# Optimization experiments

Measured on AMD Instinct MI355X. Metric: run time of the kernel, lower is better.

## Reference

```python
import jax, jax.numpy as jnp
import numpy as np

B, D = 65536, 512
E_SPEC, E_SH = 2, 2
H1, H2, EO, TH = 64, 32, 32, 64
T1_DIM, T2_DIM = 3, 2


def _lin(key, shape, fan_in):
    bound = 1.0 / np.sqrt(fan_in)
    return jax.random.uniform(key, shape, jnp.float32, -bound, bound)


def _expert_params(key, n):
    ks = jax.random.split(key, 6)
    return (
        _lin(ks[0], (n, D, H1), D), _lin(ks[1], (n, H1), D),
        _lin(ks[2], (n, H1, H2), H1), _lin(ks[3], (n, H2), H1),
        _lin(ks[4], (n, H2, EO), H2), _lin(ks[5], (n, EO), H2),
    )


def setup_inputs() -> dict:
    key = jax.random.key(0)
    ks = jax.random.split(key, 8)
    x = jax.random.normal(ks[0], (B, D), jnp.float32)
    sh = _expert_params(ks[1], E_SH)
    t1 = _expert_params(ks[2], E_SPEC)
    t2 = _expert_params(ks[3], E_SPEC)
    EG = E_SPEC + E_SH
    g1_W, g1_b = _lin(jax.random.fold_in(ks[4], 0), (D, EG), D), _lin(jax.random.fold_in(ks[4], 1), (EG,), D)
    g2_W, g2_b = _lin(jax.random.fold_in(ks[5], 0), (D, EG), D), _lin(jax.random.fold_in(ks[5], 1), (EG,), D)
    kt = jax.random.split(ks[6], 4)
    tw1_W1, tw1_b1 = _lin(kt[0], (EO, TH), EO), _lin(kt[1], (TH,), EO)
    tw1_W2, tw1_b2 = _lin(kt[2], (TH, T1_DIM), TH), _lin(kt[3], (T1_DIM,), TH)
    kt2 = jax.random.split(ks[7], 4)
    tw2_W1, tw2_b1 = _lin(kt2[0], (EO, TH), EO), _lin(kt2[1], (TH,), EO)
    tw2_W2, tw2_b2 = _lin(kt2[2], (TH, T2_DIM), TH), _lin(kt2[3], (T2_DIM,), TH)
    return {
        "x": x,
        "sh_W1": sh[0], "sh_b1": sh[1], "sh_W2": sh[2], "sh_b2": sh[3], "sh_W3": sh[4], "sh_b3": sh[5],
        "t1_W1": t1[0], "t1_b1": t1[1], "t1_W2": t1[2], "t1_b2": t1[3], "t1_W3": t1[4], "t1_b3": t1[5],
        "t2_W1": t2[0], "t2_b1": t2[1], "t2_W2": t2[2], "t2_b2": t2[3], "t2_W3": t2[4], "t2_b3": t2[5],
        "g1_W": g1_W, "g1_b": g1_b, "g2_W": g2_W, "g2_b": g2_b,
        "tw1_W1": tw1_W1, "tw1_b1": tw1_b1, "tw1_W2": tw1_W2, "tw1_b2": tw1_b2,
        "tw2_W1": tw2_W1, "tw2_b1": tw2_b1, "tw2_W2": tw2_W2, "tw2_b2": tw2_b2,
    }


def _experts(x, W1, b1, W2, b2, W3, b3):
    # batched over expert dim e: [e, B, h] (dropout is identity in eval)
    h = jax.nn.relu(jnp.einsum('bi,eih->ebh', x, W1) + b1[:, None, :])
    h = jax.nn.relu(jnp.einsum('ebh,ehk->ebk', h, W2) + b2[:, None, :])
    return jnp.einsum('ebk,eko->ebo', h, W3) + b3[:, None, :]


def _tower(g, W1, b1, W2, b2):
    return jax.nn.relu(g @ W1 + b1) @ W2 + b2


def reference(x, sh_W1, sh_b1, sh_W2, sh_b2, sh_W3, sh_b3,
              t1_W1, t1_b1, t1_W2, t1_b2, t1_W3, t1_b3,
              t2_W1, t2_b1, t2_W2, t2_b2, t2_W3, t2_b3,
              g1_W, g1_b, g2_W, g2_b,
              tw1_W1, tw1_b1, tw1_W2, tw1_b2,
              tw2_W1, tw2_b1, tw2_W2, tw2_b2):
    shared = _experts(x, sh_W1, sh_b1, sh_W2, sh_b2, sh_W3, sh_b3)   # [E_SH, B, EO]
    task1 = _experts(x, t1_W1, t1_b1, t1_W2, t1_b2, t1_W3, t1_b3)    # [E_SPEC, B, EO]
    task2 = _experts(x, t2_W1, t2_b1, t2_W2, t2_b2, t2_W3, t2_b3)

    sel1 = jax.nn.softmax(x @ g1_W + g1_b, axis=1)                    # [B, E_SPEC+E_SH]
    g1 = jnp.einsum('ebc,be->bc', jnp.concatenate([task1, shared], 0), sel1)
    o1 = _tower(g1, tw1_W1, tw1_b1, tw1_W2, tw1_b2)
    o1 = o1.at[:, 0].set(jax.nn.sigmoid(o1[:, 0]))
    o1 = o1.at[:, 2].set(jax.nn.sigmoid(o1[:, 2]))

    sel2 = jax.nn.softmax(x @ g2_W + g2_b, axis=1)
    g2 = jnp.einsum('ebc,be->bc', jnp.concatenate([task2, shared], 0), sel2)
    o2 = _tower(g2, tw2_W1, tw2_b1, tw2_W2, tw2_b2)
    o2 = o2.at[:, 1].set(jax.nn.sigmoid(o2[:, 1]))
    return (o1, o2)
```

## Files before the change

### kernel.cpp

```cpp
#include <hip/hip_runtime.h>
#include <hip/hip_bf16.h>


#define MT 64
#define NT1 25

typedef __bf16 bf16x8 __attribute__((ext_vector_type(8)));
typedef float f32x4 __attribute__((ext_vector_type(4)));

__device__ __forceinline__ unsigned short f2bf(float f) {
    unsigned u = __builtin_bit_cast(unsigned, f);
    return (unsigned short)((u + 0x7FFFu + ((u >> 16) & 1u)) >> 16);
}

__global__ void pack_w1(const float* __restrict__ sh_W1, const float* __restrict__ t1_W1,
                        const float* __restrict__ t2_W1, const float* __restrict__ g1_W,
                        const float* __restrict__ g2_W, unsigned short* __restrict__ wf1) {
    int p = blockIdx.x * blockDim.x + threadIdx.x;
    if (p >= NT1 * 16 * 64 * 8) return;
    int j = p & 7, lane = (p >> 3) & 63, ks = (p >> 9) & 15, nt = p >> 13;
    int col = nt * 16 + (lane & 15);
    int k = ks * 32 + (lane >> 4) * 8 + j;
    float v = 0.f;
    if (col < 384) {
        int e = col >> 6, ci = col & 63;
        const float* W = (e < 2) ? t1_W1 : (e < 4) ? t2_W1 : sh_W1;
        v = W[((size_t)(e & 1) * 512 + k) * 64 + ci];
    } else if (col < 388) {
        v = g1_W[k * 4 + (col - 384)];
    } else if (col < 392) {
        v = g2_W[k * 4 + (col - 388)];
    }
    wf1[p] = f2bf(v);
}

__global__ void pack_rest(const float* __restrict__ sh_W2, const float* __restrict__ t1_W2,
                          const float* __restrict__ t2_W2,
                          const float* __restrict__ sh_W3, const float* __restrict__ t1_W3,
                          const float* __restrict__ t2_W3,
                          const float* __restrict__ sh_b1, const float* __restrict__ t1_b1,
                          const float* __restrict__ t2_b1,
                          const float* __restrict__ sh_b2, const float* __restrict__ t1_b2,
                          const float* __restrict__ t2_b2,
                          const float* __restrict__ sh_b3, const float* __restrict__ t1_b3,
                          const float* __restrict__ t2_b3,
                          const float* __restrict__ g1_b, const float* __restrict__ g2_b,
                          unsigned short* __restrict__ wf2, unsigned short* __restrict__ wf3,
                          float* __restrict__ b1c, float* __restrict__ b2c, float* __restrict__ b3c) {
    int p = blockIdx.x * blockDim.x + threadIdx.x;
    if (p < 12288) {
        int j = p & 7, lane = (p >> 3) & 63, ks = (p >> 9) & 1, nt = (p >> 10) & 1, e = p >> 11;
        int col = nt * 16 + (lane & 15);
        int k = ks * 32 + (lane >> 4) * 8 + j;
        const float* W = (e < 2) ? t1_W2 : (e < 4) ? t2_W2 : sh_W2;
        wf2[p] = f2bf(W[((size_t)(e & 1) * 64 + k) * 32 + col]);
    } else if (p < 18432) {
        int q = p - 12288;
        int j = q & 7, lane = (q >> 3) & 63, nt = (q >> 9) & 1, e = q >> 10;
        int col = nt * 16 + (lane & 15);
        int k = (lane >> 4) * 8 + j;
        const float* W = (e < 2) ? t1_W3 : (e < 4) ? t2_W3 : sh_W3;
        wf3[q] = f2bf(W[((size_t)(e & 1) * 32 + k) * 32 + col]);
    } else if (p < 18432 + 392) {
        int t = p - 18432;
        float v;
        if (t < 384) {
            int e = t >> 6, ci = t & 63;
            const float* bb = (e < 2) ? t1_b1 : (e < 4) ? t2_b1 : sh_b1;
            v = bb[(e & 1) * 64 + ci];
        } else if (t < 388) v = g1_b[t - 384];
        else v = g2_b[t - 388];
        b1c[t] = v;
    } else if (p < 18824 + 192) {
        int t = p - 18824;
        int e = t >> 5, ci = t & 31;
        const float* bb = (e < 2) ? t1_b2 : (e < 4) ? t2_b2 : sh_b2;
        b2c[t] = bb[(e & 1) * 32 + ci];
    } else if (p < 19016 + 192) {
        int t = p - 19016;
        int e = t >> 5, ci = t & 31;
        const float* bb = (e < 2) ? t1_b3 : (e < 4) ? t2_b3 : sh_b3;
        b3c[t] = bb[(e & 1) * 32 + ci];
    }
}

#define LDS_BYTES 146432

__global__ __launch_bounds__(512, 2) void ple_fused(
    const float* __restrict__ x,
    const unsigned short* __restrict__ wf1, const unsigned short* __restrict__ wf2,
    const unsigned short* __restrict__ wf3,
    const float* __restrict__ b1c, const float* __restrict__ b2c, const float* __restrict__ b3c,
    const float* __restrict__ tw1_W1, const float* __restrict__ tw1_b1,
    const float* __restrict__ tw1_W2, const float* __restrict__ tw1_b2,
    const float* __restrict__ tw2_W1, const float* __restrict__ tw2_b1,
    const float* __restrict__ tw2_W2, const float* __restrict__ tw2_b2,
    float* __restrict__ out, int ntok) {
    extern __shared__ char smem[];
    unsigned short* xlds = (unsigned short*)smem;
    float* g1l = (float*)(smem + 4096);
    unsigned short* h1 = (unsigned short*)(smem + 66560);
    float* eo = (float*)(smem + 66560);
    float* th2 = (float*)(smem + 66560);
    unsigned short* h2 = (unsigned short*)(smem + 116736);
    float* g2l = (float*)(smem + 116736);
    float* th1 = (float*)(smem + 125440);
    float* gate = (float*)(smem + 142336);
    float* sel = (float*)(smem + 144384);

    const int tid = threadIdx.x;
    const int w = tid >> 6, l = tid & 63, r = l & 15, g = l >> 4;
    const int tok0 = blockIdx.x * MT;

    const float* xb = x + (size_t)tok0 * 512;
#pragma unroll
    for (int i = 0; i < 16; ++i) {
        int f = i * 2048 + tid * 4;
        const float4 v = *(const float4*)(xb + f);
        int tok = f >> 9, k = f & 511;
        unsigned lo = (unsigned)f2bf(v.x) | ((unsigned)f2bf(v.y) << 16);
        unsigned hi = (unsigned)f2bf(v.z) | ((unsigned)f2bf(v.w) << 16);
        *(uint2*)(&xlds[tok * 520 + k]) = make_uint2(lo, hi);
    }
    __syncthreads();

    int ntl[4] = {w, w + 8, w + 16, 24};
    const int ntn = (w == 7) ? 4 : 3;

    f32x4 acc[4][4];
#pragma unroll
    for (int i = 0; i < 4; ++i)
#pragma unroll
        for (int m = 0; m < 4; ++m) acc[i][m] = (f32x4){0.f, 0.f, 0.f, 0.f};

    const bf16x8* wf1v = (const bf16x8*)wf1;
#pragma unroll 4
    for (int ks = 0; ks < 16; ++ks) {
        bf16x8 bfr[4];
#pragma unroll
        for (int i = 0; i < 4; ++i)
            if (i < ntn) bfr[i] = wf1v[((ntl[i] * 16 + ks) << 6) + l];
        bf16x8 afr[4];
#pragma unroll
        for (int m = 0; m < 4; ++m)
            afr[m] = *(const bf16x8*)&xlds[(m * 16 + r) * 520 + ks * 32 + g * 8];
#pragma unroll
        for (int i = 0; i < 4; ++i)
            if (i < ntn)
#pragma unroll
                for (int m = 0; m < 4; ++m)
                    acc[i][m] = __builtin_amdgcn_mfma_f32_16x16x32_bf16(afr[m], bfr[i], acc[i][m], 0, 0, 0);
    }

#pragma unroll
    for (int i = 0; i < 4; ++i)
        if (i < ntn) {
            int nt = ntl[i];
            if (nt < 24) {
#pragma unroll
                for (int m = 0; m < 4; ++m)
#pragma unroll
                    for (int q = 0; q < 4; ++q) {
                        int tokr = m * 16 + g * 4 + q;
                        int col = nt * 16 + r;
                        float v = acc[i][m][q] + b1c[col];
                        h1[tokr * 392 + col] = f2bf(fmaxf(v, 0.f));
                    }
            } else if (r < 8) {
#pragma unroll
                for (int m = 0; m < 4; ++m)
#pragma unroll
                    for (int q = 0; q < 4; ++q) {
                        int tokr = m * 16 + g * 4 + q;
                        gate[tokr * 8 + r] = acc[i][m][q] + b1c[384 + r];
                    }
            }
        }
    __syncthreads();

    if (tid < 64) {
#pragma unroll
        for (int gi = 0; gi < 2; ++gi) {
            float l0 = gate[tid * 8 + gi * 4 + 0];
            float l1 = gate[tid * 8 + gi * 4 + 1];
            float l2 = gate[tid * 8 + gi * 4 + 2];
            float l3 = gate[tid * 8 + gi * 4 + 3];
            float mx = fmaxf(fmaxf(l0, l1), fmaxf(l2, l3));
            float e0 = __expf(l0 - mx), e1 = __expf(l1 - mx);
            float e2 = __expf(l2 - mx), e3 = __expf(l3 - mx);
            float inv = 1.f / (e0 + e1 + e2 + e3);
            sel[tid * 8 + gi * 4 + 0] = e0 * inv;
            sel[tid * 8 + gi * 4 + 1] = e1 * inv;
            sel[tid * 8 + gi * 4 + 2] = e2 * inv;
            sel[tid * 8 + gi * 4 + 3] = e3 * inv;
        }
    }

    const int nj = (w < 4) ? 2 : 1;
    const int je[2] = {w >> 1, (w + 8) >> 1};
    const int jn[2] = {w & 1, w & 1};

    f32x4 acc2[2][4];
#pragma unroll
    for (int jj = 0; jj < 2; ++jj)
#pragma unroll
        for (int m = 0; m < 4; ++m) acc2[jj][m] = (f32x4){0.f, 0.f, 0.f, 0.f};

    const bf16x8* wf2v = (const bf16x8*)wf2;
#pragma unroll
    for (int jj = 0; jj < 2; ++jj)
        if (jj < nj) {
            int e = je[jj], nt2 = jn[jj];
#pragma unroll
            for (int ks = 0; ks < 2; ++ks) {
                bf16x8 bb = wf2v[(((e * 2 + nt2) * 2 + ks) << 6) + l];
#pragma unroll
                for (int m = 0; m < 4; ++m) {
                    bf16x8 aa = *(const bf16x8*)&h1[(m * 16 + r) * 392 + e * 64 + ks * 32 + g * 8];
                    acc2[jj][m] = __builtin_amdgcn_mfma_f32_16x16x32_bf16(aa, bb, acc2[jj][m], 0, 0, 0);
                }
            }
        }
#pragma unroll
    for (int jj = 0; jj < 2; ++jj)
        if (jj < nj) {
            int e = je[jj], nt2 = jn[jj];
#pragma unroll
            for (int m = 0; m < 4; ++m)
#pragma unroll
                for (int q = 0; q < 4; ++q) {
                    int tokr = m * 16 + g * 4 + q;
                    int col = nt2 * 16 + r;
                    float v = acc2[jj][m][q] + b2c[e * 32 + col];
                    h2[tokr * 200 + e * 32 + col] = f2bf(fmaxf(v, 0.f));
                }
        }
    __syncthreads();

    f32x4 acc3[2][4];
#pragma unroll
    for (int jj = 0; jj < 2; ++jj)
#pragma unroll
        for (int m = 0; m < 4; ++m) acc3[jj][m] = (f32x4){0.f, 0.f, 0.f, 0.f};

    const bf16x8* wf3v = (const bf16x8*)wf3;
#pragma unroll
    for (int jj = 0; jj < 2; ++jj)
        if (jj < nj) {
            int e = je[jj], nt2 = jn[jj];
            bf16x8 bb = wf3v[((e * 2 + nt2) << 6) + l];
#pragma unroll
            for (int m = 0; m < 4; ++m) {
                bf16x8 aa = *(const bf16x8*)&h2[(m * 16 + r) * 200 + e * 32 + g * 8];
                acc3[jj][m] = __builtin_amdgcn_mfma_f32_16x16x32_bf16(aa, bb, acc3[jj][m], 0, 0, 0);
            }
        }
#pragma unroll
    for (int jj = 0; jj < 2; ++jj)
        if (jj < nj) {
            int e = je[jj], nt2 = jn[jj];
#pragma unroll
            for (int m = 0; m < 4; ++m)
#pragma unroll
                for (int q = 0; q < 4; ++q) {
                    int tokr = m * 16 + g * 4 + q;
                    eo[((size_t)e * 64 + tokr) * 32 + nt2 * 16 + r] =
                        acc3[jj][m][q] + b3c[e * 32 + nt2 * 16 + r];
                }
        }
    __syncthreads();

    {
        int tok = tid >> 3, c0 = (tid & 7) * 4;
        float s[8];
#pragma unroll
        for (int i = 0; i < 8; ++i) s[i] = sel[tok * 8 + i];
#pragma unroll
        for (int c = 0; c < 4; ++c) {
            int cc = c0 + c;
            float e0 = eo[((size_t)0 * 64 + tok) * 32 + cc];
            float e1 = eo[((size_t)1 * 64 + tok) * 32 + cc];
            float e2 = eo[((size_t)2 * 64 + tok) * 32 + cc];
            float e3 = eo[((size_t)3 * 64 + tok) * 32 + cc];
            float e4 = eo[((size_t)4 * 64 + tok) * 32 + cc];
            float e5 = eo[((size_t)5 * 64 + tok) * 32 + cc];
            g1l[tok * 34 + cc] = s[0] * e0 + s[1] * e1 + s[2] * e4 + s[3] * e5;
            g2l[tok * 34 + cc] = s[4] * e2 + s[5] * e3 + s[6] * e4 + s[7] * e5;
        }
    }
    __syncthreads();

    {
        int tok = tid >> 3, h0 = (tid & 7) * 8;
        float a1[8], a2[8];
#pragma unroll
        for (int hh = 0; hh < 8; ++hh) {
            a1[hh] = tw1_b1[h0 + hh];
            a2[hh] = tw2_b1[h0 + hh];
        }
        for (int c = 0; c < 32; ++c) {
            float gv1 = g1l[tok * 34 + c], gv2 = g2l[tok * 34 + c];
#pragma unroll
            for (int hh = 0; hh < 8; ++hh) {
                a1[hh] += gv1 * tw1_W1[c * 64 + h0 + hh];
                a2[hh] += gv2 * tw2_W1[c * 64 + h0 + hh];
            }
        }
#pragma unroll
        for (int hh = 0; hh < 8; ++hh) {
            th1[tok * 66 + h0 + hh] = fmaxf(a1[hh], 0.f);
            th2[tok * 66 + h0 + hh] = fmaxf(a2[hh], 0.f);
        }
    }
    __syncthreads();

    if (tid < 192) {
        int tok = tid / 3, jx = tid % 3;
        float s = tw1_b2[jx];
        for (int hh = 0; hh < 64; ++hh) s += th1[tok * 66 + hh] * tw1_W2[hh * 3 + jx];
        if (jx != 1) s = 1.f / (1.f + __expf(-s));
        out[(size_t)(tok0 + tok) * 3 + jx] = s;
    } else if (tid < 320) {
        int t2 = tid - 192, tok = t2 >> 1, jx = t2 & 1;
        float s = tw2_b2[jx];
        for (int hh = 0; hh < 64; ++hh) s += th2[tok * 66 + hh] * tw2_W2[hh * 2 + jx];
        if (jx == 1) s = 1.f / (1.f + __expf(-s));
        out[(size_t)ntok * 3 + (size_t)(tok0 + tok) * 2 + jx] = s;
    }
}

extern "C" void kernel_launch(void* const* d_in, const int* in_sizes, int n_in,
                              void* d_out, int out_size, void* d_ws, size_t ws_size,
                              hipStream_t stream) {
    const float* x = (const float*)d_in[0];
    const float* sh_W1 = (const float*)d_in[1];
    const float* sh_b1 = (const float*)d_in[2];
    const float* sh_W2 = (const float*)d_in[3];
    const float* sh_b2 = (const float*)d_in[4];
    const float* sh_W3 = (const float*)d_in[5];
    const float* sh_b3 = (const float*)d_in[6];
    const float* t1_W1 = (const float*)d_in[7];
    const float* t1_b1 = (const float*)d_in[8];
    const float* t1_W2 = (const float*)d_in[9];
    const float* t1_b2 = (const float*)d_in[10];
    const float* t1_W3 = (const float*)d_in[11];
    const float* t1_b3 = (const float*)d_in[12];
    const float* t2_W1 = (const float*)d_in[13];
    const float* t2_b1 = (const float*)d_in[14];
    const float* t2_W2 = (const float*)d_in[15];
    const float* t2_b2 = (const float*)d_in[16];
    const float* t2_W3 = (const float*)d_in[17];
    const float* t2_b3 = (const float*)d_in[18];
    const float* g1_W = (const float*)d_in[19];
    const float* g1_b = (const float*)d_in[20];
    const float* g2_W = (const float*)d_in[21];
    const float* g2_b = (const float*)d_in[22];
    const float* tw1_W1 = (const float*)d_in[23];
    const float* tw1_b1 = (const float*)d_in[24];
    const float* tw1_W2 = (const float*)d_in[25];
    const float* tw1_b2 = (const float*)d_in[26];
    const float* tw2_W1 = (const float*)d_in[27];
    const float* tw2_b1 = (const float*)d_in[28];
    const float* tw2_W2 = (const float*)d_in[29];
    const float* tw2_b2 = (const float*)d_in[30];

    unsigned short* wf1 = (unsigned short*)d_ws;
    unsigned short* wf2 = (unsigned short*)((char*)d_ws + 409600);
    unsigned short* wf3 = (unsigned short*)((char*)d_ws + 434176);
    float* b1c = (float*)((char*)d_ws + 446464);
    float* b2c = (float*)((char*)d_ws + 448032);
    float* b3c = (float*)((char*)d_ws + 448800);

    pack_w1<<<400, 512, 0, stream>>>(sh_W1, t1_W1, t2_W1, g1_W, g2_W, wf1);
    pack_rest<<<38, 512, 0, stream>>>(sh_W2, t1_W2, t2_W2, sh_W3, t1_W3, t2_W3,
                                      sh_b1, t1_b1, t2_b1, sh_b2, t1_b2, t2_b2,
                                      sh_b3, t1_b3, t2_b3, g1_b, g2_b,
                                      wf2, wf3, b1c, b2c, b3c);

    (void)hipFuncSetAttribute((const void*)ple_fused,
                              hipFuncAttributeMaxDynamicSharedMemorySize, LDS_BYTES);

    int ntok = in_sizes[0] / 512;
    int nblk = ntok / MT;
    ple_fused<<<nblk, 512, LDS_BYTES, stream>>>(
        x, wf1, wf2, wf3, b1c, b2c, b3c,
        tw1_W1, tw1_b1, tw1_W2, tw1_b2, tw2_W1, tw2_b1, tw2_W2, tw2_b2,
        (float*)d_out, ntok);
}
```

Baseline: 331.1 us.

## Halve token tile to 32 and repack LDS for four blocks per CU

Cuts the per-block token tile from 64 to 32, shrinks and reorganises the LDS layout so four 512-thread blocks can be resident per CU, and halves the accumulator register footprint. It also merges the two weight-packing kernels into one launch, widens the x load/convert to 8 floats per thread, pads the h1 and expert-output strides, and splits the tower computation across thread halves. The aim is higher occupancy and latency hiding plus one fewer launch. The trade-off is that each weight fragment from global memory is now reused over half as many tokens, so weight traffic per token doubles.

```diff
diff --git a/kernel.cpp b/kernel.cpp
--- a/kernel.cpp
+++ b/kernel.cpp
@@ -2,7 +2,7 @@
 #include <hip/hip_bf16.h>
 
 
-#define MT 64
+#define MT 32
 #define NT1 25
 
 typedef __bf16 bf16x8 __attribute__((ext_vector_type(8)));
@@ -12,42 +12,47 @@
     unsigned u = __builtin_bit_cast(unsigned, f);
     return (unsigned short)((u + 0x7FFFu + ((u >> 16) & 1u)) >> 16);
 }
-
-__global__ void pack_w1(const float* __restrict__ sh_W1, const float* __restrict__ t1_W1,
-                        const float* __restrict__ t2_W1, const float* __restrict__ g1_W,
-                        const float* __restrict__ g2_W, unsigned short* __restrict__ wf1) {
-    int p = blockIdx.x * blockDim.x + threadIdx.x;
-    if (p >= NT1 * 16 * 64 * 8) return;
-    int j = p & 7, lane = (p >> 3) & 63, ks = (p >> 9) & 15, nt = p >> 13;
-    int col = nt * 16 + (lane & 15);
-    int k = ks * 32 + (lane >> 4) * 8 + j;
-    float v = 0.f;
-    if (col < 384) {
-        int e = col >> 6, ci = col & 63;
-        const float* W = (e < 2) ? t1_W1 : (e < 4) ? t2_W1 : sh_W1;
-        v = W[((size_t)(e & 1) * 512 + k) * 64 + ci];
-    } else if (col < 388) {
-        v = g1_W[k * 4 + (col - 384)];
-    } else if (col < 392) {
-        v = g2_W[k * 4 + (col - 388)];
-    }
-    wf1[p] = f2bf(v);
-}
-
-__global__ void pack_rest(const float* __restrict__ sh_W2, const float* __restrict__ t1_W2,
-                          const float* __restrict__ t2_W2,
-                          const float* __restrict__ sh_W3, const float* __restrict__ t1_W3,
-                          const float* __restrict__ t2_W3,
-                          const float* __restrict__ sh_b1, const float* __restrict__ t1_b1,
-                          const float* __restrict__ t2_b1,
-                          const float* __restrict__ sh_b2, const float* __restrict__ t1_b2,
-                          const float* __restrict__ t2_b2,
-                          const float* __restrict__ sh_b3, const float* __restrict__ t1_b3,
-                          const float* __restrict__ t2_b3,
-                          const float* __restrict__ g1_b, const float* __restrict__ g2_b,
-                          unsigned short* __restrict__ wf2, unsigned short* __restrict__ wf3,
-                          float* __restrict__ b1c, float* __restrict__ b2c, float* __restrict__ b3c) {
-    int p = blockIdx.x * blockDim.x + threadIdx.x;
+__device__ __forceinline__ unsigned pk(float a, float b) {
+    return (unsigned)f2bf(a) | ((unsigned)f2bf(b) << 16);
+}
+
+__global__ void pack_all(const float* __restrict__ sh_W1, const float* __restrict__ t1_W1,
+                         const float* __restrict__ t2_W1, const float* __restrict__ g1_W,
+                         const float* __restrict__ g2_W,
+                         const float* __restrict__ sh_W2, const float* __restrict__ t1_W2,
+                         const float* __restrict__ t2_W2,
+                         const float* __restrict__ sh_W3, const float* __restrict__ t1_W3,
+                         const float* __restrict__ t2_W3,
+                         const float* __restrict__ sh_b1, const float* __restrict__ t1_b1,
+                         const float* __restrict__ t2_b1,
+                         const float* __restrict__ sh_b2, const float* __restrict__ t1_b2,
+                         const float* __restrict__ t2_b2,
+                         const float* __restrict__ sh_b3, const float* __restrict__ t1_b3,
+                         const float* __restrict__ t2_b3,
+                         const float* __restrict__ g1_b, const float* __restrict__ g2_b,
+                         unsigned short* __restrict__ wf1, unsigned short* __restrict__ wf2,
+                         unsigned short* __restrict__ wf3,
+                         float* __restrict__ b1c, float* __restrict__ b2c, float* __restrict__ b3c) {
+    int p0 = blockIdx.x * blockDim.x + threadIdx.x;
+    if (p0 < 204800) {
+        int p = p0;
+        int j = p & 7, lane = (p >> 3) & 63, ks = (p >> 9) & 15, nt = p >> 13;
+        int col = nt * 16 + (lane & 15);
+        int k = ks * 32 + (lane >> 4) * 8 + j;
+        float v = 0.f;
+        if (col < 384) {
+            int e = col >> 6, ci = col & 63;
+            const float* W = (e < 2) ? t1_W1 : (e < 4) ? t2_W1 : sh_W1;
+            v = W[((size_t)(e & 1) * 512 + k) * 64 + ci];
+        } else if (col < 388) {
+            v = g1_W[k * 4 + (col - 384)];
+        } else if (col < 392) {
+            v = g2_W[k * 4 + (col - 388)];
+        }
+        wf1[p] = f2bf(v);
+        return;
+    }
+    int p = p0 - 204800;
     if (p < 12288) {
         int j = p & 7, lane = (p >> 3) & 63, ks = (p >> 9) & 1, nt = (p >> 10) & 1, e = p >> 11;
         int col = nt * 16 + (lane & 15);
@@ -84,9 +89,9 @@
     }
 }
 
-#define LDS_BYTES 146432
-
-__global__ __launch_bounds__(512, 2) void ple_fused(
+#define LDS_BYTES 74240
+
+__global__ __launch_bounds__(512, 4) void ple_fused(
     const float* __restrict__ x,
     const unsigned short* __restrict__ wf1, const unsigned short* __restrict__ wf2,
     const unsigned short* __restrict__ wf3,
@@ -98,15 +103,15 @@
     float* __restrict__ out, int ntok) {
     extern __shared__ char smem[];
     unsigned short* xlds = (unsigned short*)smem;
-    float* g1l = (float*)(smem + 4096);
-    unsigned short* h1 = (unsigned short*)(smem + 66560);
-    float* eo = (float*)(smem + 66560);
-    float* th2 = (float*)(smem + 66560);
-    unsigned short* h2 = (unsigned short*)(smem + 116736);
-    float* g2l = (float*)(smem + 116736);
-    float* th1 = (float*)(smem + 125440);
-    float* gate = (float*)(smem + 142336);
-    float* sel = (float*)(smem + 144384);
+    float* g1l = (float*)(smem + 0);
+    float* g2l = (float*)(smem + 4224);
+    float* th1 = (float*)(smem + 8448);
+    float* th2 = (float*)(smem + 16896);
+    unsigned short* h1 = (unsigned short*)(smem + 33280);
+    float* eo = (float*)(smem + 33280);
+    unsigned short* h2 = (unsigned short*)(smem + 59392);
+    float* gate = (float*)(smem + 72192);
+    float* sel = (float*)(smem + 73216);
 
     const int tid = threadIdx.x;
     const int w = tid >> 6, l = tid & 63, r = l & 15, g = l >> 4;
@@ -114,24 +119,24 @@
 
     const float* xb = x + (size_t)tok0 * 512;
 #pragma unroll
-    for (int i = 0; i < 16; ++i) {
-        int f = i * 2048 + tid * 4;
-        const float4 v = *(const float4*)(xb + f);
+    for (int i = 0; i < 4; ++i) {
+        int f = i * 4096 + tid * 8;
+        const float4 a = *(const float4*)(xb + f);
+        const float4 b = *(const float4*)(xb + f + 4);
         int tok = f >> 9, k = f & 511;
-        unsigned lo = (unsigned)f2bf(v.x) | ((unsigned)f2bf(v.y) << 16);
-        unsigned hi = (unsigned)f2bf(v.z) | ((unsigned)f2bf(v.w) << 16);
-        *(uint2*)(&xlds[tok * 520 + k]) = make_uint2(lo, hi);
+        uint4 u = make_uint4(pk(a.x, a.y), pk(a.z, a.w), pk(b.x, b.y), pk(b.z, b.w));
+        *(uint4*)(&xlds[tok * 520 + k]) = u;
     }
     __syncthreads();
 
     int ntl[4] = {w, w + 8, w + 16, 24};
     const int ntn = (w == 7) ? 4 : 3;
 
-    f32x4 acc[4][4];
+    f32x4 acc[4][2];
 #pragma unroll
     for (int i = 0; i < 4; ++i)
 #pragma unroll
-        for (int m = 0; m < 4; ++m) acc[i][m] = (f32x4){0.f, 0.f, 0.f, 0.f};
+        for (int m = 0; m < 2; ++m) acc[i][m] = (f32x4){0.f, 0.f, 0.f, 0.f};
 
     const bf16x8* wf1v = (const bf16x8*)wf1;
 #pragma unroll 4
@@ -140,15 +145,15 @@
 #pragma unroll
         for (int i = 0; i < 4; ++i)
             if (i < ntn) bfr[i] = wf1v[((ntl[i] * 16 + ks) << 6) + l];
-        bf16x8 afr[4];
-#pragma unroll
-        for (int m = 0; m < 4; ++m)
+        bf16x8 afr[2];
+#pragma unroll
+        for (int m = 0; m < 2; ++m)
             afr[m] = *(const bf16x8*)&xlds[(m * 16 + r) * 520 + ks * 32 + g * 8];
 #pragma unroll
         for (int i = 0; i < 4; ++i)
             if (i < ntn)
 #pragma unroll
-                for (int m = 0; m < 4; ++m)
+                for (int m = 0; m < 2; ++m)
                     acc[i][m] = __builtin_amdgcn_mfma_f32_16x16x32_bf16(afr[m], bfr[i], acc[i][m], 0, 0, 0);
     }
 
@@ -158,17 +163,17 @@
             int nt = ntl[i];
             if (nt < 24) {
 #pragma unroll
-                for (int m = 0; m < 4; ++m)
+                for (int m = 0; m < 2; ++m)
 #pragma unroll
                     for (int q = 0; q < 4; ++q) {
                         int tokr = m * 16 + g * 4 + q;
                         int col = nt * 16 + r;
                         float v = acc[i][m][q] + b1c[col];
-                        h1[tokr * 392 + col] = f2bf(fmaxf(v, 0.f));
+                        h1[tokr * 408 + col] = f2bf(fmaxf(v, 0.f));
                     }
             } else if (r < 8) {
 #pragma unroll
-                for (int m = 0; m < 4; ++m)
+                for (int m = 0; m < 2; ++m)
 #pragma unroll
                     for (int q = 0; q < 4; ++q) {
                         int tokr = m * 16 + g * 4 + q;
@@ -178,7 +183,7 @@
         }
     __syncthreads();
 
-    if (tid < 64) {
+    if (tid < 32) {
 #pragma unroll
         for (int gi = 0; gi < 2; ++gi) {
             float l0 = gate[tid * 8 + gi * 4 + 0];
@@ -200,11 +205,11 @@
     const int je[2] = {w >> 1, (w + 8) >> 1};
     const int jn[2] = {w & 1, w & 1};
 
-    f32x4 acc2[2][4];
-#pragma unroll
-    for (int jj = 0; jj < 2; ++jj)
-#pragma unroll
-        for (int m = 0; m < 4; ++m) acc2[jj][m] = (f32x4){0.f, 0.f, 0.f, 0.f};
+    f32x4 acc2[2][2];
+#pragma unroll
+    for (int jj = 0; jj < 2; ++jj)
+#pragma unroll
+        for (int m = 0; m < 2; ++m) acc2[jj][m] = (f32x4){0.f, 0.f, 0.f, 0.f};
 
     const bf16x8* wf2v = (const bf16x8*)wf2;
 #pragma unroll
@@ -215,8 +220,8 @@
             for (int ks = 0; ks < 2; ++ks) {
                 bf16x8 bb = wf2v[(((e * 2 + nt2) * 2 + ks) << 6) + l];
 #pragma unroll
-                for (int m = 0; m < 4; ++m) {
-                    bf16x8 aa = *(const bf16x8*)&h1[(m * 16 + r) * 392 + e * 64 + ks * 32 + g * 8];
+                for (int m = 0; m < 2; ++m) {
+                    bf16x8 aa = *(const bf16x8*)&h1[(m * 16 + r) * 408 + e * 64 + ks * 32 + g * 8];
                     acc2[jj][m] = __builtin_amdgcn_mfma_f32_16x16x32_bf16(aa, bb, acc2[jj][m], 0, 0, 0);
                 }
             }
@@ -226,7 +231,7 @@
         if (jj < nj) {
             int e = je[jj], nt2 = jn[jj];
 #pragma unroll
-            for (int m = 0; m < 4; ++m)
+            for (int m = 0; m < 2; ++m)
 #pragma unroll
                 for (int q = 0; q < 4; ++q) {
                     int tokr = m * 16 + g * 4 + q;
@@ -237,11 +242,11 @@
         }
     __syncthreads();
 
-    f32x4 acc3[2][4];
-#pragma unroll
-    for (int jj = 0; jj < 2; ++jj)
-#pragma unroll
-        for (int m = 0; m < 4; ++m) acc3[jj][m] = (f32x4){0.f, 0.f, 0.f, 0.f};
+    f32x4 acc3[2][2];
+#pragma unroll
+    for (int jj = 0; jj < 2; ++jj)
+#pragma unroll
+        for (int m = 0; m < 2; ++m) acc3[jj][m] = (f32x4){0.f, 0.f, 0.f, 0.f};
 
     const bf16x8* wf3v = (const bf16x8*)wf3;
 #pragma unroll
@@ -250,7 +255,7 @@
             int e = je[jj], nt2 = jn[jj];
             bf16x8 bb = wf3v[((e * 2 + nt2) << 6) + l];
 #pragma unroll
-            for (int m = 0; m < 4; ++m) {
+            for (int m = 0; m < 2; ++m) {
                 bf16x8 aa = *(const bf16x8*)&h2[(m * 16 + r) * 200 + e * 32 + g * 8];
                 acc3[jj][m] = __builtin_amdgcn_mfma_f32_16x16x32_bf16(aa, bb, acc3[jj][m], 0, 0, 0);
             }
@@ -260,72 +265,74 @@
         if (jj < nj) {
             int e = je[jj], nt2 = jn[jj];
 #pragma unroll
-            for (int m = 0; m < 4; ++m)
+            for (int m = 0; m < 2; ++m)
 #pragma unroll
                 for (int q = 0; q < 4; ++q) {
                     int tokr = m * 16 + g * 4 + q;
-                    eo[((size_t)e * 64 + tokr) * 32 + nt2 * 16 + r] =
+                    eo[(e * 32 + tokr) * 33 + nt2 * 16 + r] =
                         acc3[jj][m][q] + b3c[e * 32 + nt2 * 16 + r];
                 }
         }
     __syncthreads();
 
     {
-        int tok = tid >> 3, c0 = (tid & 7) * 4;
+        int tok = tid >> 4, c0 = (tid & 15) * 2;
         float s[8];
 #pragma unroll
         for (int i = 0; i < 8; ++i) s[i] = sel[tok * 8 + i];
 #pragma unroll
-        for (int c = 0; c < 4; ++c) {
+        for (int c = 0; c < 2; ++c) {
             int cc = c0 + c;
-            float e0 = eo[((size_t)0 * 64 + tok) * 32 + cc];
-            float e1 = eo[((size_t)1 * 64 + tok) * 32 + cc];
-            float e2 = eo[((size_t)2 * 64 + tok) * 32 + cc];
-            float e3 = eo[((size_t)3 * 64 + tok) * 32 + cc];
-            float e4 = eo[((size_t)4 * 64 + tok) * 32 + cc];
-            float e5 = eo[((size_t)5 * 64 + tok) * 32 + cc];
-            g1l[tok * 34 + cc] = s[0] * e0 + s[1] * e1 + s[2] * e4 + s[3] * e5;
-            g2l[tok * 34 + cc] = s[4] * e2 + s[5] * e3 + s[6] * e4 + s[7] * e5;
+            float e0 = eo[(0 * 32 + tok) * 33 + cc];
+            float e1 = eo[(1 * 32 + tok) * 33 + cc];
+            float e2 = eo[(2 * 32 + tok) * 33 + cc];
+            float e3 = eo[(3 * 32 + tok) * 33 + cc];
+            float e4 = eo[(4 * 32 + tok) * 33 + cc];
+            float e5 = eo[(5 * 32 + tok) * 33 + cc];
+            g1l[tok * 33 + cc] = s[0] * e0 + s[1] * e1 + s[2] * e4 + s[3] * e5;
+            g2l[tok * 33 + cc] = s[4] * e2 + s[5] * e3 + s[6] * e4 + s[7] * e5;
         }
     }
     __syncthreads();
 
     {
-        int tok = tid >> 3, h0 = (tid & 7) * 8;
-        float a1[8], a2[8];
-#pragma unroll
-        for (int hh = 0; hh < 8; ++hh) {
-            a1[hh] = tw1_b1[h0 + hh];
-            a2[hh] = tw2_b1[h0 + hh];
-        }
+        int t = tid & 255, tower = tid >> 8;
+        int tok = t >> 3, h0 = (t & 7) * 8;
+        const float* W1 = tower ? tw2_W1 : tw1_W1;
+        const float* B1 = tower ? tw2_b1 : tw1_b1;
+        const float* gl = tower ? g2l : g1l;
+        float* th = tower ? th2 : th1;
+        float a[8];
+#pragma unroll
+        for (int hh = 0; hh < 8; ++hh) a[hh] = B1[h0 + hh];
         for (int c = 0; c < 32; ++c) {
-            float gv1 = g1l[tok * 34 + c], gv2 = g2l[tok * 34 + c];
-#pragma unroll
-            for (int hh = 0; hh < 8; ++hh) {
-                a1[hh] += gv1 * tw1_W1[c * 64 + h0 + hh];
-                a2[hh] += gv2 * tw2_W1[c * 64 + h0 + hh];
-            }
-        }
-#pragma unroll
-        for (int hh = 0; hh < 8; ++hh) {
-            th1[tok * 66 + h0 + hh] = fmaxf(a1[hh], 0.f);
-            th2[tok * 66 + h0 + hh] = fmaxf(a2[hh], 0.f);
-        }
-    }
-    __syncthreads();
-
-    if (tid < 192) {
-        int tok = tid / 3, jx = tid % 3;
-        float s = tw1_b2[jx];
-        for (int hh = 0; hh < 64; ++hh) s += th1[tok * 66 + hh] * tw1_W2[hh * 3 + jx];
-        if (jx != 1) s = 1.f / (1.f + __expf(-s));
-        out[(size_t)(tok0 + tok) * 3 + jx] = s;
-    } else if (tid < 320) {
-        int t2 = tid - 192, tok = t2 >> 1, jx = t2 & 1;
-        float s = tw2_b2[jx];
-        for (int hh = 0; hh < 64; ++hh) s += th2[tok * 66 + hh] * tw2_W2[hh * 2 + jx];
-        if (jx == 1) s = 1.f / (1.f + __expf(-s));
-        out[(size_t)ntok * 3 + (size_t)(tok0 + tok) * 2 + jx] = s;
+            float gv = gl[tok * 33 + c];
+#pragma unroll
+            for (int hh = 0; hh < 8; ++hh)
+                a[hh] += gv * W1[c * 64 + h0 + hh];
+        }
+#pragma unroll
+        for (int hh = 0; hh < 8; ++hh)
+            th[tok * 66 + h0 + hh] = fmaxf(a[hh], 0.f);
+    }
+    __syncthreads();
+
+    if (tid < 128) {
+        int tok = tid >> 2, jx = tid & 3;
+        if (jx < 3) {
+            float s = tw1_b2[jx];
+            for (int hh = 0; hh < 64; ++hh) s += th1[tok * 66 + hh] * tw1_W2[hh * 3 + jx];
+            if (jx != 1) s = 1.f / (1.f + __expf(-s));
+            out[(size_t)(tok0 + tok) * 3 + jx] = s;
+        }
+    } else if (tid >= 256 && tid < 384) {
+        int t = tid - 256, tok = t >> 2, jx = t & 3;
+        if (jx < 2) {
+            float s = tw2_b2[jx];
+            for (int hh = 0; hh < 64; ++hh) s += th2[tok * 66 + hh] * tw2_W2[hh * 2 + jx];
+            if (jx == 1) s = 1.f / (1.f + __expf(-s));
+            out[(size_t)ntok * 3 + (size_t)(tok0 + tok) * 2 + jx] = s;
+        }
     }
 }
 
@@ -371,11 +378,11 @@
     float* b2c = (float*)((char*)d_ws + 448032);
     float* b3c = (float*)((char*)d_ws + 448800);
 
-    pack_w1<<<400, 512, 0, stream>>>(sh_W1, t1_W1, t2_W1, g1_W, g2_W, wf1);
-    pack_rest<<<38, 512, 0, stream>>>(sh_W2, t1_W2, t2_W2, sh_W3, t1_W3, t2_W3,
+    pack_all<<<438, 512, 0, stream>>>(sh_W1, t1_W1, t2_W1, g1_W, g2_W,
+                                      sh_W2, t1_W2, t2_W2, sh_W3, t1_W3, t2_W3,
                                       sh_b1, t1_b1, t2_b1, sh_b2, t1_b2, t2_b2,
                                       sh_b3, t1_b3, t2_b3, g1_b, g2_b,
-                                      wf2, wf3, b1c, b2c, b3c);
+                                      wf1, wf2, wf3, b1c, b2c, b3c);
 
     (void)hipFuncSetAttribute((const void*)ple_fused,
                               hipFuncAttributeMaxDynamicSharedMemorySize, LDS_BYTES);
```

After: 306.9 us. -7.3%, faster.
